# Optimization experiments

Hardware: AMD Instinct MI355X
Metric: run time of the kernel (lower is better)

## Reference

```python
import jax, jax.numpy as jnp
import numpy as np

DIM = 768
NUM_HEADS = 12
HEAD_DIM = DIM // NUM_HEADS
WS = 14                       # window_size (14, 14)
N_TOK = WS * WS + 1           # 197 (patches + cls)
NUM_REL = (2 * WS - 1) ** 2 + 3  # 732
SCALE = HEAD_DIM ** -0.5


def _build_rel_index():
    # Faithful port of the BEiT relative_position_index construction.
    coords = np.stack(np.meshgrid(np.arange(WS), np.arange(WS), indexing='ij'))  # (2, WS, WS)
    flat = coords.reshape(2, -1)                                   # (2, WS*WS)
    rel = flat[:, :, None] - flat[:, None, :]                      # (2, P, P)
    rel = rel.transpose(1, 2, 0).astype(np.int64)                  # (P, P, 2)
    rel[:, :, 0] += WS - 1
    rel[:, :, 1] += WS - 1
    rel[:, :, 0] *= 2 * WS - 1
    idx = np.zeros((N_TOK, N_TOK), dtype=np.int64)
    idx[1:, 1:] = rel.sum(-1)
    idx[0, :] = NUM_REL - 3
    idx[:, 0] = NUM_REL - 2
    idx[0, 0] = NUM_REL - 1
    return idx


def setup_inputs() -> dict:
    key = jax.random.key(0)
    ks = jax.random.split(key, 7)
    B = 64
    x = jax.random.normal(ks[0], (B, N_TOK, DIM), dtype=jnp.float32)
    qkv_w = jax.random.normal(ks[1], (3 * DIM, DIM), dtype=jnp.float32) * 0.02
    q_bias = jnp.zeros((DIM,), dtype=jnp.float32)
    v_bias = jnp.zeros((DIM,), dtype=jnp.float32)
    rel_table = jax.random.normal(ks[2], (NUM_REL, NUM_HEADS), dtype=jnp.float32) * 0.02
    proj_w = jax.random.normal(ks[3], (DIM, DIM), dtype=jnp.float32) * 0.02
    proj_b = jnp.zeros((DIM,), dtype=jnp.float32)
    rel_index = jnp.asarray(_build_rel_index())  # (N, N) int64
    return {"x": x, "qkv_w": qkv_w, "q_bias": q_bias, "v_bias": v_bias,
            "rel_table": rel_table, "proj_w": proj_w, "proj_b": proj_b,
            "rel_index": rel_index}


def reference(x, qkv_w, q_bias, v_bias, rel_table, proj_w, proj_b, rel_index):
    B, N, C = x.shape
    # qkv bias = concat(q_bias, zeros, v_bias)
    qkv_b = jnp.concatenate([q_bias, jnp.zeros_like(v_bias), v_bias])
    qkv = x @ qkv_w.T + qkv_b                       # (B, N, 3C)
    qkv = qkv.reshape(B, N, 3, NUM_HEADS, HEAD_DIM).transpose(2, 0, 3, 1, 4)
    q, k, v = qkv[0], qkv[1], qkv[2]                # each (B, H, N, hd)
    attn = jnp.einsum('bhqd,bhkd->bhqk', q * SCALE, k)
    # relative position bias gathered from table: (N, N, H) -> (H, N, N)
    bias = rel_table[rel_index].transpose(2, 0, 1)
    attn = attn + bias[None]
    attn = jax.nn.softmax(attn, axis=-1)
    out = jnp.einsum('bhqk,bhkd->bhqd', attn, v)    # (B, H, N, hd)
    out = out.transpose(0, 2, 1, 3).reshape(B, N, -1)
    return out @ proj_w.T + proj_b
```

## Files before the change

### kernel.cpp

```cpp
#include <hip/hip_runtime.h>
#include <stdint.h>

#define NTOK 197
#define HD 64
#define NH 12
#define CDIM 768
#define BB 64
#define MTOT (BB*NTOK)
#define MPAD 12672
#define SCALE 0.125f

typedef __attribute__((ext_vector_type(8))) short short8;
typedef __attribute__((ext_vector_type(4))) float f32x4;
typedef unsigned short us;

__device__ __forceinline__ us f2b(float f){
    union { float f; uint32_t u; } v; v.f = f;
    uint32_t u = v.u;
    uint32_t r = u + 0x7fffu + ((u >> 16) & 1u);
    return (us)(r >> 16);
}

__device__ __forceinline__ float b2f(us b){
    union { uint32_t u; float f; } v; v.u = ((uint32_t)b) << 16;
    return v.f;
}

__device__ __forceinline__ void gload16(const us* g, us* l){
    __builtin_amdgcn_global_load_lds((const __attribute__((address_space(1))) void*)g,
                                     (__attribute__((address_space(3))) void*)l, 16, 0, 0);
}

#define LGKM0_BAR() do{ asm volatile("s_waitcnt lgkmcnt(0)" ::: "memory"); \
                        __builtin_amdgcn_s_barrier(); }while(0)

__global__ void cvt_kernel(const float* __restrict__ in, us* __restrict__ out, int n4){
    int i = blockIdx.x*blockDim.x + threadIdx.x;
    if (i < n4){
        float4 v = ((const float4*)in)[i];
        ushort4 o;
        o.x = f2b(v.x); o.y = f2b(v.y); o.z = f2b(v.z); o.w = f2b(v.w);
        ((ushort4*)out)[i] = o;
    }
}

__global__ void bias_kernel(const int* __restrict__ rel_index, const float* __restrict__ rel_table,
                            float* __restrict__ biasm){
    int i = blockIdx.x*blockDim.x + threadIdx.x;
    if (i < NTOK*NTOK){
        int idx = rel_index[i];
        #pragma unroll
        for (int h = 0; h < NH; ++h)
            biasm[h*NTOK*NTOK + i] = rel_table[idx*NH + h];
    }
}

__global__ __launch_bounds__(512,1) void pgemm3_kernel(
    const us* __restrict__ A, const us* __restrict__ Bw,
    us* __restrict__ Qo, us* __restrict__ Ko, us* __restrict__ Vo,
    const float* __restrict__ b0, const float* __restrict__ b2, int ny, int total)
{
    __shared__ __align__(16) us AsB[2][24576];
    __shared__ __align__(16) us cbuf[128*132];
    const int tid  = threadIdx.x;
    const int lane = tid & 63;
    const int wave = tid >> 6;
    const int wrr = wave >> 2;
    const int wcc = wave & 3;
    const int lr = lane & 15;
    const int g  = lane >> 4;

    const int id  = blockIdx.x;
    const int xcd = id & 7;
    const int jb  = id >> 3;
    const int qs  = total >> 3, rs = total & 7;
    const int Ssp = xcd*qs + (xcd < rs ? xcd : rs);
    const int L   = qs + (xcd < rs ? 1 : 0);
    const int qb  = L >> 5, rb = L & 31;
    const int cnt = qb + (jb < rb ? 1 : 0);
    const int w0  = Ssp + jb*qb + (jb < rb ? jb : rb);
    if (cnt == 0) return;

    int aoff[2], bofs[4];
    int aldo[2], bldo[4];
    #pragma unroll
    for (int p=0;p<2;p++){
        int c = tid + p*512;
        int row = c >> 3, ch = c & 7;
        aoff[p] = row*CDIM + ((ch ^ (row & 7))*8);
        aldo[p] = c*8;
    }
    #pragma unroll
    for (int jj=0;jj<4;jj++){
        int c = tid + jj*512;
        int row = c >> 3, ch = c & 7;
        bofs[jj] = row*CDIM + ((ch ^ (row & 7))*8);
        bldo[jj] = 8192 + c*8;
    }

    const int S = cnt * 12;
    auto stageStep = [&](int x){
        int tt = x / 12, kt = x - tt*12;
        int ww = w0 + tt;
        int bx = ww / ny, by = ww - bx*ny;
        const us* pA = A  + (size_t)(bx*128)*CDIM;
        const us* pB = Bw + (size_t)(by*256)*CDIM;
        int buf = x & 1;
        #pragma unroll
        for (int p=0;p<2;p++) gload16(pA + aoff[p] + kt*64, &AsB[buf][aldo[p]]);
        #pragma unroll
        for (int jj=0;jj<4;jj++) gload16(pB + bofs[jj] + kt*64, &AsB[buf][bldo[jj]]);
    };

    stageStep(0);
    if (S > 1) stageStep(1);
    int s = 0;

    #pragma unroll 1
    for (int tt = 0; tt < cnt; ++tt){
        const int w  = w0 + tt;
        const int bx = w / ny, by = w - bx*ny;
        const int m0 = bx*128, n0 = by*256;
        const int whc = n0 / CDIM;
        float addf[4];
        const float sclf = (whc == 0) ? SCALE : 1.f;
        #pragma unroll
        for (int nt=0;nt<4;nt++){
            int n = n0 + wcc*64 + nt*16 + lr;
            int hn = n - whc*CDIM;
            addf[nt] = (whc == 0) ? b0[hn] : (whc == 2 ? b2[hn] : 0.f);
        }

        f32x4 acc[4][4];
        #pragma unroll
        for (int i=0;i<4;i++)
            #pragma unroll
            for (int jj=0;jj<4;jj++) acc[i][jj] = (f32x4){0.f,0.f,0.f,0.f};

        #pragma unroll 1
        for (int kt = 0; kt < 12; ++kt){
            if (s == S-1) asm volatile("s_waitcnt vmcnt(0)" ::: "memory");
            else          asm volatile("s_waitcnt vmcnt(6)" ::: "memory");
            __builtin_amdgcn_s_barrier();
            const us* la = &AsB[s & 1][0];
            const us* lb = &AsB[s & 1][8192];
            #pragma unroll
            for (int kk=0; kk<2; ++kk){
                const int co = 8*((kk*4 + g) ^ (lr & 7));
                short8 af[4], bf[4];
                #pragma unroll
                for (int mt=0;mt<4;mt++)
                    af[mt] = *(const short8*)&la[(wrr*64+mt*16+lr)*64 + co];
                #pragma unroll
                for (int nt=0;nt<4;nt++)
                    bf[nt] = *(const short8*)&lb[(wcc*64+nt*16+lr)*64 + co];
                __builtin_amdgcn_s_setprio(1);
                #pragma unroll
                for (int mt=0;mt<4;mt++)
                    #pragma unroll
                    for (int nt=0;nt<4;nt++)
                        acc[mt][nt] = __builtin_amdgcn_mfma_f32_16x16x32_bf16(af[mt], bf[nt], acc[mt][nt], 0,0,0);
                __builtin_amdgcn_s_setprio(0);
            }
            LGKM0_BAR();
            if (s + 2 < S) stageStep(s + 2);
            ++s;
        }

        const us* outp = (whc == 0 ? Qo : (whc == 1 ? Ko : Vo));
        #pragma unroll 1
        for (int half = 0; half < 2; ++half){
            if ((wcc >> 1) == half){
                #pragma unroll
                for (int mt=0;mt<4;mt++)
                    #pragma unroll
                    for (int rr=0;rr<4;rr++){
                        int row = wrr*64 + mt*16 + g*4 + rr;
                        #pragma unroll
                        for (int nt=0;nt<4;nt++){
                            int col = (wcc & 1)*64 + nt*16 + lr;
                            cbuf[row*132 + col] = f2b((acc[mt][nt][rr] + addf[nt]) * sclf);
                        }
                    }
            }
            LGKM0_BAR();
            #pragma unroll
            for (int p=0;p<4;p++){
                int c = tid + p*512;
                int row = c >> 4, ch = c & 15;
                int m = m0 + row;
                if (m < MTOT){
                    short8 vv = *(const short8*)&cbuf[row*132 + ch*8];
                    int n = n0 + half*128 + ch*8;
                    int hn = n - whc*CDIM;
                    int h  = hn >> 6, d0 = hn & 63;
                    int bidx = m / NTOK;
                    int tok  = m - bidx*NTOK;
                    size_t off = ((size_t)((bidx*NH + h)*NTOK + tok))*HD + d0;
                    *(short8*)((us*)outp + off) = vv;
                }
            }
            LGKM0_BAR();
        }
    }
}

__global__ __launch_bounds__(256) void proj_gemm_kernel(
    const us* __restrict__ A, const us* __restrict__ Bw,
    float* __restrict__ Cout, const float* __restrict__ b0, int ny)
{
    __shared__ __align__(16) us lds[32768];
    us* As = lds;
    us* Bs = lds + 16384;
    const int tid  = threadIdx.x;
    const int lane = tid & 63;
    const int wave = tid >> 6;
    const int wr = wave >> 1, wc = wave & 1;
    const int lr = lane & 15;
    const int g  = lane >> 4;

    const int NB   = gridDim.x;
    const int base = NB >> 3;
    const int rem  = NB & 7;
    const int id   = blockIdx.x;
    const int xcd  = id & 7;
    const int qq   = id >> 3;
    const int start = (xcd < rem) ? xcd*(base+1) : rem*(base+1) + (xcd-rem)*base;
    const int w    = start + qq;
    const int bx   = w / ny;
    const int by   = w - bx*ny;
    const int m0 = bx * 128;
    const int n0 = by * 128;
    const int NT = CDIM / 128;

    const int row0 = tid >> 4;
    const int cg   = (tid & 15) ^ row0;

    float addf[4];
    #pragma unroll
    for (int nt=0;nt<4;nt++) addf[nt] = b0[n0 + wc*64 + nt*16 + lr];

    f32x4 acc[4][4];
    #pragma unroll
    for (int i=0;i<4;i++)
        #pragma unroll
        for (int j=0;j<4;j++) acc[i][j] = (f32x4){0.f,0.f,0.f,0.f};

    const us* gA = A  + (size_t)(m0 + row0)*CDIM + cg*8;
    const us* gB = Bw + (size_t)(n0 + row0)*CDIM + cg*8;

    #pragma unroll 1
    for (int kt = 0; kt < NT; ++kt){
        __syncthreads();
        #pragma unroll
        for (int j=0;j<8;j++){
            gload16(gA + (size_t)j*16*CDIM + kt*128, As + tid*8 + j*2048);
            gload16(gB + (size_t)j*16*CDIM + kt*128, Bs + tid*8 + j*2048);
        }
        __syncthreads();
        #pragma unroll
        for (int kk=0; kk<4; ++kk){
            const int co = 8*((kk*4 + g) ^ lr);
            short8 af[4], bf[4];
            #pragma unroll
            for (int mt=0;mt<4;mt++)
                af[mt] = *(const short8*)&As[(wr*64+mt*16+lr)*128 + co];
            #pragma unroll
            for (int nt=0;nt<4;nt++)
                bf[nt] = *(const short8*)&Bs[(wc*64+nt*16+lr)*128 + co];
            __builtin_amdgcn_s_setprio(1);
            #pragma unroll
            for (int mt=0;mt<4;mt++)
                #pragma unroll
                for (int nt=0;nt<4;nt++)
                    acc[mt][nt] = __builtin_amdgcn_mfma_f32_16x16x32_bf16(af[mt], bf[nt], acc[mt][nt], 0,0,0);
            __builtin_amdgcn_s_setprio(0);
        }
    }

    __syncthreads();
    #pragma unroll
    for (int mt=0;mt<4;mt++)
        #pragma unroll
        for (int r=0;r<4;r++){
            int row = wr*64 + mt*16 + g*4 + r;
            #pragma unroll
            for (int nt=0;nt<4;nt++){
                int col = wc*64 + nt*16 + lr;
                lds[row*132 + col] = f2b(acc[mt][nt][r] + addf[nt]);
            }
        }
    __syncthreads();
    #pragma unroll
    for (int j=0;j<8;j++){
        int c2  = tid + j*256;
        int row = c2 >> 4;
        int ch  = c2 & 15;
        int m = m0 + row;
        if (m >= MTOT) continue;
        short8 vv = *(const short8*)&lds[row*132 + ch*8];
        int n = n0 + ch*8;
        float4 f0, f1;
        f0.x = b2f((us)vv[0]); f0.y = b2f((us)vv[1]); f0.z = b2f((us)vv[2]); f0.w = b2f((us)vv[3]);
        f1.x = b2f((us)vv[4]); f1.y = b2f((us)vv[5]); f1.z = b2f((us)vv[6]); f1.w = b2f((us)vv[7]);
        *(float4*)&Cout[(size_t)m*CDIM + n]     = f0;
        *(float4*)&Cout[(size_t)m*CDIM + n + 4] = f1;
    }
}

__global__ __launch_bounds__(256) void attn_kernel(
    const us* __restrict__ Q,
    const us* __restrict__ K,
    const us* __restrict__ V,
    const float* __restrict__ biasm,
    us* __restrict__ Ao)
{
    __shared__ us Vt[64][232];
    __shared__ us Ps[4][16][232];
    const int bh = blockIdx.x;
    const int b = bh / NH;
    const int h = bh - b*NH;
    const us* Qh = Q + (size_t)bh*NTOK*HD;
    const us* Kh = K + (size_t)bh*NTOK*HD;
    const us* Vh = V + (size_t)bh*NTOK*HD;
    const float* bh_bias = biasm + (size_t)h*NTOK*NTOK;
    const int tid = threadIdx.x, lane = tid & 63, wave = tid >> 6;
    const int lr = lane & 15, g = lane >> 4, ko = g*8;

    for (int i = tid; i < 64*232/2; i += 256) ((uint32_t*)Vt)[i] = 0;
    __syncthreads();
    {
        int d0 = (tid & 7) * 8;
        for (int t = tid >> 3; t < NTOK; t += 32){
            short8 v = *(const short8*)&Vh[t*HD + d0];
            #pragma unroll
            for (int j=0;j<8;j++) Vt[d0+j][t] = (us)v[j];
        }
    }
    __syncthreads();

    for (int s = wave; s < 13; s += 4){
        int qrow = s*16 + lr; qrow = qrow > 196 ? 196 : qrow;
        short8 qa0 = *(const short8*)&Qh[qrow*HD + ko];
        short8 qa1 = *(const short8*)&Qh[qrow*HD + 32 + ko];
        f32x4 S[13];
        #pragma unroll
        for (int t=0;t<13;t++){
            int kc = t*16 + lr; kc = kc > 196 ? 196 : kc;
            short8 kb0 = *(const short8*)&Kh[kc*HD + ko];
            short8 kb1 = *(const short8*)&Kh[kc*HD + 32 + ko];
            f32x4 a = (f32x4){0.f,0.f,0.f,0.f};
            a = __builtin_amdgcn_mfma_f32_16x16x32_bf16(qa0, kb0, a, 0,0,0);
            a = __builtin_amdgcn_mfma_f32_16x16x32_bf16(qa1, kb1, a, 0,0,0);
            S[t] = a;
        }
        float rmax[4] = {-3e38f,-3e38f,-3e38f,-3e38f};
        #pragma unroll
        for (int t=0;t<13;t++){
            int col = t*16 + lr;
            bool cok = col < NTOK;
            int colc = cok ? col : 196;
            #pragma unroll
            for (int r=0;r<4;r++){
                int row = s*16 + g*4 + r; row = row > 196 ? 196 : row;
                float xv = S[t][r] + bh_bias[row*NTOK + colc];
                xv = cok ? xv : -1e30f;
                S[t][r] = xv;
                rmax[r] = fmaxf(rmax[r], xv);
            }
        }
        #pragma unroll
        for (int r=0;r<4;r++)
            #pragma unroll
            for (int msk=1; msk<16; msk<<=1)
                rmax[r] = fmaxf(rmax[r], __shfl_xor(rmax[r], msk));
        float rsum[4] = {0.f,0.f,0.f,0.f};
        #pragma unroll
        for (int t=0;t<13;t++)
            #pragma unroll
            for (int r=0;r<4;r++){
                float e = __expf(S[t][r] - rmax[r]);
                S[t][r] = e;
                rsum[r] += e;
            }
        #pragma unroll
        for (int r=0;r<4;r++){
            #pragma unroll
            for (int msk=1; msk<16; msk<<=1)
                rsum[r] += __shfl_xor(rsum[r], msk);
            rsum[r] = 1.f / rsum[r];
        }
        #pragma unroll
        for (int t=0;t<13;t++)
            #pragma unroll
            for (int r=0;r<4;r++)
                Ps[wave][g*4+r][t*16+lr] = f2b(S[t][r] * rsum[r]);
        #pragma unroll
        for (int r=0;r<4;r++) Ps[wave][g*4+r][208+lr] = 0;
        asm volatile("s_waitcnt lgkmcnt(0)" ::: "memory");
        f32x4 pv[4];
        #pragma unroll
        for (int nt=0;nt<4;nt++) pv[nt] = (f32x4){0.f,0.f,0.f,0.f};
        #pragma unroll
        for (int ks=0; ks<7; ks++){
            int k0 = ks*32 + ko;
            short8 pa = *(const short8*)&Ps[wave][lr][k0];
            #pragma unroll
            for (int nt=0;nt<4;nt++){
                short8 vb = *(const short8*)&Vt[nt*16+lr][k0];
                pv[nt] = __builtin_amdgcn_mfma_f32_16x16x32_bf16(pa, vb, pv[nt], 0,0,0);
            }
        }
        #pragma unroll
        for (int nt=0;nt<4;nt++)
            #pragma unroll
            for (int r=0;r<4;r++){
                int tok = s*16 + g*4 + r;
                if (tok < NTOK)
                    Ao[(size_t)(b*NTOK + tok)*CDIM + h*HD + nt*16 + lr] = f2b(pv[nt][r]);
            }
    }
}

extern "C" void kernel_launch(void* const* d_in, const int* in_sizes, int n_in,
                              void* d_out, int out_size, void* d_ws, size_t ws_size,
                              hipStream_t stream)
{
    const float* x        = (const float*)d_in[0];
    const float* qkv_w    = (const float*)d_in[1];
    const float* q_bias   = (const float*)d_in[2];
    const float* v_bias   = (const float*)d_in[3];
    const float* rel_tab  = (const float*)d_in[4];
    const float* proj_w   = (const float*)d_in[5];
    const float* proj_b   = (const float*)d_in[6];
    const int*   rel_idx  = (const int*)d_in[7];
    float* out = (float*)d_out;

    char* w = (char*)d_ws;
    us* xb    = (us*)w; w += (size_t)MPAD*CDIM*2;
    us* wqkv  = (us*)w; w += (size_t)3*CDIM*CDIM*2;
    us* wproj = (us*)w; w += (size_t)CDIM*CDIM*2;
    us* Qb    = (us*)w; w += (size_t)BB*NH*NTOK*HD*2;
    us* Kb    = (us*)w; w += (size_t)BB*NH*NTOK*HD*2;
    us* Vb    = (us*)w; w += (size_t)BB*NH*NTOK*HD*2;
    float* biasm = (float*)w; w += (size_t)NH*NTOK*NTOK*4;
    us* aob   = (us*)w; w += (size_t)MPAD*CDIM*2;

    int n1 = MTOT*CDIM/4;
    cvt_kernel<<<(n1+255)/256, 256, 0, stream>>>(x, xb, n1);
    int n2 = 3*CDIM*CDIM/4;
    cvt_kernel<<<(n2+255)/256, 256, 0, stream>>>(qkv_w, wqkv, n2);
    int n3 = CDIM*CDIM/4;
    cvt_kernel<<<(n3+255)/256, 256, 0, stream>>>(proj_w, wproj, n3);
    bias_kernel<<<(NTOK*NTOK+255)/256, 256, 0, stream>>>(rel_idx, rel_tab, biasm);

    pgemm3_kernel<<<256, 512, 0, stream>>>(xb, wqkv, Qb, Kb, Vb, q_bias, v_bias, 9, 891);
    attn_kernel<<<BB*NH, 256, 0, stream>>>(Qb, Kb, Vb, biasm, aob);
    proj_gemm_kernel<<<594, 256, 0, stream>>>(aob, wproj, out, proj_b, 6);
}
```

Before: 175.3 us.

## Fuse conversion and bias prep kernels; store padded transposed bias for vector loads

```diff
diff --git a/kernel.cpp b/kernel.cpp
--- a/kernel.cpp
+++ b/kernel.cpp
@@ -9,6 +9,7 @@
 #define MTOT (BB*NTOK)
 #define MPAD 12672
 #define SCALE 0.125f
+#define BTP 208
 
 typedef __attribute__((ext_vector_type(8))) short short8;
 typedef __attribute__((ext_vector_type(4))) float f32x4;
@@ -34,24 +35,42 @@
 #define LGKM0_BAR() do{ asm volatile("s_waitcnt lgkmcnt(0)" ::: "memory"); \
                         __builtin_amdgcn_s_barrier(); }while(0)
 
-__global__ void cvt_kernel(const float* __restrict__ in, us* __restrict__ out, int n4){
-    int i = blockIdx.x*blockDim.x + threadIdx.x;
-    if (i < n4){
-        float4 v = ((const float4*)in)[i];
-        ushort4 o;
-        o.x = f2b(v.x); o.y = f2b(v.y); o.z = f2b(v.z); o.w = f2b(v.w);
-        ((ushort4*)out)[i] = o;
-    }
-}
-
-__global__ void bias_kernel(const int* __restrict__ rel_index, const float* __restrict__ rel_table,
-                            float* __restrict__ biasm){
-    int i = blockIdx.x*blockDim.x + threadIdx.x;
-    if (i < NTOK*NTOK){
-        int idx = rel_index[i];
-        #pragma unroll
-        for (int h = 0; h < NH; ++h)
-            biasm[h*NTOK*NTOK + i] = rel_table[idx*NH + h];
+__device__ __forceinline__ void cvt4(const float* in, us* out, int i){
+    float4 v = ((const float4*)in)[i];
+    ushort4 o;
+    o.x = f2b(v.x); o.y = f2b(v.y); o.z = f2b(v.z); o.w = f2b(v.w);
+    ((ushort4*)out)[i] = o;
+}
+
+__global__ void prep_kernel(const float* __restrict__ x, const float* __restrict__ qkv_w,
+                            const float* __restrict__ proj_w,
+                            const int* __restrict__ rel_index, const float* __restrict__ rel_table,
+                            us* __restrict__ xb, us* __restrict__ wqkv, us* __restrict__ wproj,
+                            float* __restrict__ biasT)
+{
+    const int N1 = MTOT*CDIM/4;
+    const int N2 = 3*CDIM*CDIM/4;
+    const int N3 = CDIM*CDIM/4;
+    const int N4 = BTP*BTP;
+    const int total = N1+N2+N3+N4;
+    for (int i = blockIdx.x*blockDim.x + threadIdx.x; i < total; i += gridDim.x*blockDim.x){
+        if (i < N1) cvt4(x, xb, i);
+        else if (i < N1+N2) cvt4(qkv_w, wqkv, i-N1);
+        else if (i < N1+N2+N3) cvt4(proj_w, wproj, i-N1-N2);
+        else {
+            int t = i - N1 - N2 - N3;
+            int col = t / BTP, row = t - col*BTP;
+            if (row < NTOK && col < NTOK){
+                int idx = rel_index[row*NTOK + col];
+                #pragma unroll
+                for (int h = 0; h < NH; ++h)
+                    biasT[((size_t)h*BTP + col)*BTP + row] = rel_table[idx*NH + h];
+            } else {
+                #pragma unroll
+                for (int h = 0; h < NH; ++h)
+                    biasT[((size_t)h*BTP + col)*BTP + row] = 0.f;
+            }
+        }
     }
 }
 
@@ -312,7 +331,7 @@
     const us* __restrict__ Q,
     const us* __restrict__ K,
     const us* __restrict__ V,
-    const float* __restrict__ biasm,
+    const float* __restrict__ biasT,
     us* __restrict__ Ao)
 {
     __shared__ us Vt[64][232];
@@ -323,7 +342,7 @@
     const us* Qh = Q + (size_t)bh*NTOK*HD;
     const us* Kh = K + (size_t)bh*NTOK*HD;
     const us* Vh = V + (size_t)bh*NTOK*HD;
-    const float* bh_bias = biasm + (size_t)h*NTOK*NTOK;
+    const float* bT = biasT + (size_t)h*BTP*BTP;
     const int tid = threadIdx.x, lane = tid & 63, wave = tid >> 6;
     const int lr = lane & 15, g = lane >> 4, ko = g*8;
 
@@ -359,11 +378,10 @@
         for (int t=0;t<13;t++){
             int col = t*16 + lr;
             bool cok = col < NTOK;
-            int colc = cok ? col : 196;
+            float4 b4 = *(const float4*)&bT[(size_t)col*BTP + s*16 + g*4];
             #pragma unroll
             for (int r=0;r<4;r++){
-                int row = s*16 + g*4 + r; row = row > 196 ? 196 : row;
-                float xv = S[t][r] + bh_bias[row*NTOK + colc];
+                float xv = S[t][r] + ((const float*)&b4)[r];
                 xv = cok ? xv : -1e30f;
                 S[t][r] = xv;
                 rmax[r] = fmaxf(rmax[r], xv);
@@ -443,18 +461,13 @@
     us* Qb    = (us*)w; w += (size_t)BB*NH*NTOK*HD*2;
     us* Kb    = (us*)w; w += (size_t)BB*NH*NTOK*HD*2;
     us* Vb    = (us*)w; w += (size_t)BB*NH*NTOK*HD*2;
-    float* biasm = (float*)w; w += (size_t)NH*NTOK*NTOK*4;
+    float* biasT = (float*)w; w += (size_t)NH*BTP*BTP*4;
     us* aob   = (us*)w; w += (size_t)MPAD*CDIM*2;
 
-    int n1 = MTOT*CDIM/4;
-    cvt_kernel<<<(n1+255)/256, 256, 0, stream>>>(x, xb, n1);
-    int n2 = 3*CDIM*CDIM/4;
-    cvt_kernel<<<(n2+255)/256, 256, 0, stream>>>(qkv_w, wqkv, n2);
-    int n3 = CDIM*CDIM/4;
-    cvt_kernel<<<(n3+255)/256, 256, 0, stream>>>(proj_w, wproj, n3);
-    bias_kernel<<<(NTOK*NTOK+255)/256, 256, 0, stream>>>(rel_idx, rel_tab, biasm);
+    prep_kernel<<<2048, 256, 0, stream>>>(x, qkv_w, proj_w, rel_idx, rel_tab,
+                                          xb, wqkv, wproj, biasT);
 
     pgemm3_kernel<<<256, 512, 0, stream>>>(xb, wqkv, Qb, Kb, Vb, q_bias, v_bias, 9, 891);
-    attn_kernel<<<BB*NH, 256, 0, stream>>>(Qb, Kb, Vb, biasm, aob);
+    attn_kernel<<<BB*NH, 256, 0, stream>>>(Qb, Kb, Vb, biasT, aob);
     proj_gemm_kernel<<<594, 256, 0, stream>>>(aob, wproj, out, proj_b, 6);
 }
```

After: 169.1 us. -3.5%, faster.
